# Performance work log

Measured on AMD Instinct MI355X. Metric: run time of the kernel, lower is better.

## Reference

```python
import jax, jax.numpy as jnp
import numpy as np

N = 100_000   # nodes
E = 1_600_000 # edges
G, H1, H2, Z = 64, 64, 64, 32


def _w(k, o, i):
    return jax.random.normal(k, (o, i), jnp.float32) * (1.0 / np.sqrt(i))


def setup_inputs() -> dict:
    key = jax.random.key(0)
    ks = jax.random.split(key, 16)
    inp = {
        "x": jax.random.normal(ks[0], (N, G), jnp.float32),
        "edge_src": jax.random.randint(ks[1], (E,), 0, N, jnp.int32),
        "edge_dst": jax.random.randint(ks[2], (E,), 0, N, jnp.int32),
        "eps": jax.random.normal(ks[3], (N, Z), jnp.float32),
        "W1": _w(ks[4], H1, G),  "b1": jnp.zeros((H1,), jnp.float32),
        "W2": _w(ks[5], H2, H1), "b2": jnp.zeros((H2,), jnp.float32),
        "W31": _w(ks[6], Z, H2), "b31": jnp.zeros((Z,), jnp.float32),
        "W32": _w(ks[7], Z, H2), "b32": jnp.zeros((Z,), jnp.float32),
        "W4": _w(ks[8], H2, Z),  "b4": jnp.zeros((H2,), jnp.float32),
        "W5": _w(ks[9], H1, H2), "b5": jnp.zeros((H1,), jnp.float32),
        "W6": _w(ks[10], G, H1), "b6": jnp.zeros((G,), jnp.float32),
    }
    return inp


def _gcn(h, W, b, act, src, dst, norm):
    # message: h_src * norm_src, gathered per edge  [E, d]
    m = (h * norm)[src]
    # reduce: sum over incoming edges, scaled by norm_dst  [N, d]
    agg = jax.ops.segment_sum(m, dst, num_segments=N) * norm
    # node apply: linear + activation
    return act(agg @ W.T + b)


def reference(x, edge_src, edge_dst, eps,
              W1, b1, W2, b2, W31, b31, W32, b32, W4, b4, W5, b5, W6, b6):
    # symmetric GCN norm: deg^{-1/2} from in-degree
    deg = jax.ops.segment_sum(jnp.ones((E,), jnp.float32), edge_dst, num_segments=N)
    norm = jax.lax.rsqrt(jnp.maximum(deg, 1.0))[:, None]  # [N,1]

    relu = jax.nn.relu
    ident = lambda h: h

    h = _gcn(x, W1, b1, relu, edge_src, edge_dst, norm)
    h = _gcn(h, W2, b2, relu, edge_src, edge_dst, norm)
    mu = _gcn(h, W31, b31, ident, edge_src, edge_dst, norm)
    log_var = _gcn(h, W32, b32, ident, edge_src, edge_dst, norm)

    z = eps * jnp.exp(0.5 * log_var) + mu

    h = _gcn(z, W4, b4, relu, edge_src, edge_dst, norm)
    h = _gcn(h, W5, b5, relu, edge_src, edge_dst, norm)
    recon = _gcn(h, W6, b6, jax.nn.sigmoid, edge_src, edge_dst, norm)
    return recon, mu, log_var
```

## Files before the change

kernel.cpp:

```cpp
#include <hip/hip_runtime.h>
#include <hip/hip_fp16.h>
#include <math.h>

#define NN 100000
#define NE 1600000
#define NBKT 391
#define CHUNK 8192
#define NB1 ((NE + CHUNK - 1) / CHUNK)
#define QSEG 25000
#define NNP (NN + 8)
#define CAP 5120

typedef _Float16 v8h __attribute__((ext_vector_type(8)));
typedef float v4f __attribute__((ext_vector_type(4)));

union H4 { uint2 u; __half2 h[2]; };

__global__ __launch_bounds__(256) void p1_scatter_kernel(const int* __restrict__ src,
                                                         const int* __restrict__ dst,
                                                         int* __restrict__ bcnt,
                                                         int* __restrict__ gpair) {
    __shared__ int h[NBKT], rb[NBKT], hc[NBKT];
    int tid = threadIdx.x;
    for (int b = tid; b < NBKT; b += 256) { h[b] = 0; hc[b] = 0; }
    __syncthreads();
    int e0 = blockIdx.x * CHUNK;
    for (int k = 0; k < CHUNK / 256; ++k) {
        int e = e0 + tid + k * 256;
        if (e < NE) atomicAdd(&h[dst[e] >> 8], 1);
    }
    __syncthreads();
    for (int b = tid; b < NBKT; b += 256)
        rb[b] = h[b] ? atomicAdd(&bcnt[b], h[b]) : 0;
    __syncthreads();
    for (int k = 0; k < CHUNK / 256; ++k) {
        int e = e0 + tid + k * 256;
        if (e < NE) {
            int d = dst[e], s = src[e];
            int b = d >> 8;
            int pos = b * CAP + rb[b] + atomicAdd(&hc[b], 1);
            gpair[pos] = (s << 8) | (d & 255);
        }
    }
}

__global__ __launch_bounds__(256) void p2_place_kernel(const int* __restrict__ gpair,
                                                       const int* __restrict__ bcnt,
                                                       int* __restrict__ csr,
                                                       int* __restrict__ seg,
                                                       float* __restrict__ nrm,
                                                       const float4* __restrict__ x4,
                                                       uint2* __restrict__ xs) {
    __shared__ int cseg[4][256], nexcl[256], sb[4][256], pq[4][256];
    __shared__ float nrmS[256];
    int b = blockIdx.x, tid = threadIdx.x;
    int s0 = b * CAP, s1 = s0 + bcnt[b];
#pragma unroll
    for (int q = 0; q < 4; ++q) { cseg[q][tid] = 0; pq[q][tid] = 0; }
    __syncthreads();
    for (int i = s0 + tid; i < s1; i += 256) {
        int p = gpair[i];
        int l = p & 255;
        int q = (p >> 8) / QSEG;
        atomicAdd(&cseg[q][l], 1);
    }
    __syncthreads();
    int v = cseg[0][tid] + cseg[1][tid] + cseg[2][tid] + cseg[3][tid];
    nexcl[tid] = v;
    __syncthreads();
    for (int off = 1; off < 256; off <<= 1) {
        int t = (tid >= off) ? nexcl[tid - off] : 0;
        __syncthreads();
        nexcl[tid] += t;
        __syncthreads();
    }
    int ex = nexcl[tid] - v;
    int base = s0 + ex;
    int node = (b << 8) + tid;
    int c0 = cseg[0][tid], c1 = cseg[1][tid], c2 = cseg[2][tid];
    float nv = rsqrtf(fmaxf((float)v, 1.0f));
    if (node < NN) {
        seg[0 * NNP + node] = base;
        seg[1 * NNP + node] = base + c0;
        seg[2 * NNP + node] = base + c0 + c1;
        seg[3 * NNP + node] = base + c0 + c1 + c2;
        seg[4 * NNP + node] = base + v;
        nrm[node] = nv;
    }
    nrmS[tid] = nv;
    sb[0][tid] = base;
    sb[1][tid] = base + c0;
    sb[2][tid] = base + c0 + c1;
    sb[3][tid] = base + c0 + c1 + c2;
    __syncthreads();
    for (int i = s0 + tid; i < s1; i += 256) {
        int p = gpair[i];
        int l = p & 255;
        int s = p >> 8;
        int q = s / QSEG;
        int pos = sb[q][l] + atomicAdd(&pq[q][l], 1);
        csr[pos] = s;
    }
    int nbase = b << 8;
    int nvalid = NN - nbase; if (nvalid > 256) nvalid = 256;
    for (int idx = tid; idx < nvalid * 16; idx += 256) {
        int nl = idx >> 4, f = idx & 15;
        float s = nrmS[nl];
        float4 xv = x4[(size_t)(nbase + nl) * 16 + f];
        H4 w;
        w.h[0] = __floats2half2_rn(xv.x * s, xv.y * s);
        w.h[1] = __floats2half2_rn(xv.z * s, xv.w * s);
        xs[(size_t)(nbase + nl) * 16 + f] = w.u;
    }
}

template<int IN, int ACT, bool SCALE, bool DUAL>
__global__ __launch_bounds__(256) void gcn_layer_kernel(
        const __half* __restrict__ h,
        const float* __restrict__ nrm,
        const int* __restrict__ seg,
        const int* __restrict__ csr,
        const float* __restrict__ Wa, const float* __restrict__ ba,
        const float* __restrict__ Wb, const float* __restrict__ bb,
        void* __restrict__ outv, float* __restrict__ out2,
        const float* __restrict__ eps, __half* __restrict__ zbuf) {
    constexpr int MLP = 8;
    constexpr int RL  = IN / 4;
    constexpr int EPI = 64 / RL;
    constexpr int KH  = IN / 32;
    constexpr int AS  = IN + 8;
    constexpr int HS  = 72;
    constexpr int FS  = 68;
    constexpr int MS  = 36;
    constexpr int OUTB = DUAL ? (2 * 32 * MS * 4) : (SCALE ? 32 * HS * 2 : 32 * FS * 4);
    __shared__ __half aggH[32 * AS];
    __shared__ __align__(16) char smem[OUTB];

    int tid = threadIdx.x;
    int wave = tid >> 6, lane = tid & 63;
    int row_slot = lane / RL;
    int f4 = lane % RL;
    int nodeBase = (blockIdx.x * 4 + wave) * MLP;
    const uint2* hp = (const uint2*)h;

    float4 acc[MLP];
#pragma unroll
    for (int i = 0; i < MLP; ++i) acc[i] = make_float4(0.f, 0.f, 0.f, 0.f);

    int cur[MLP];
#pragma unroll
    for (int i = 0; i < MLP; ++i) cur[i] = seg[nodeBase + i];

    for (int q = 0; q < 4; ++q) {
        int nxt[MLP];
#pragma unroll
        for (int i = 0; i < MLP; ++i) nxt[i] = seg[(q + 1) * NNP + nodeBase + i];
        int maxd = 0;
#pragma unroll
        for (int i = 0; i < MLP; ++i) maxd = max(maxd, nxt[i] - cur[i]);

        for (int t = 0; t < maxd; t += EPI) {
            int s[MLP]; float m[MLP];
#pragma unroll
            for (int i = 0; i < MLP; ++i) {
                int jj = cur[i] + t + row_slot;
                bool ok = jj < nxt[i];
                s[i] = csr[ok ? jj : 0];
                m[i] = ok ? 1.f : 0.f;
            }
            H4 v[MLP];
#pragma unroll
            for (int i = 0; i < MLP; ++i)
                v[i].u = hp[(size_t)s[i] * RL + f4];
#pragma unroll
            for (int i = 0; i < MLP; ++i) {
                float2 f01 = __half22float2(v[i].h[0]);
                float2 f23 = __half22float2(v[i].h[1]);
                acc[i].x = fmaf(m[i], f01.x, acc[i].x);
                acc[i].y = fmaf(m[i], f01.y, acc[i].y);
                acc[i].z = fmaf(m[i], f23.x, acc[i].z);
                acc[i].w = fmaf(m[i], f23.y, acc[i].w);
            }
        }
#pragma unroll
        for (int i = 0; i < MLP; ++i) cur[i] = nxt[i];
    }

#pragma unroll
    for (int i = 0; i < MLP; ++i) {
        for (int o = RL; o < 64; o <<= 1) {
            acc[i].x += __shfl_xor(acc[i].x, o);
            acc[i].y += __shfl_xor(acc[i].y, o);
            acc[i].z += __shfl_xor(acc[i].z, o);
            acc[i].w += __shfl_xor(acc[i].w, o);
        }
    }

    if (row_slot == 0) {
#pragma unroll
        for (int i = 0; i < MLP; ++i) {
            H4 w;
            w.h[0] = __floats2half2_rn(acc[i].x, acc[i].y);
            w.h[1] = __floats2half2_rn(acc[i].z, acc[i].w);
            *(uint2*)&aggH[(wave * MLP + i) * AS + f4 * 4] = w.u;
        }
    }

    int col = lane & 15, kgrp = lane >> 4;
    v8h Bhi[KH], Blo[KH];
    float bias;
    {
        const float* wrow;
        if (DUAL) wrow = (wave < 2) ? (Wa + (size_t)(wave * 16 + col) * 64)
                                    : (Wb + (size_t)((wave - 2) * 16 + col) * 64);
        else      wrow = Wa + (size_t)(wave * 16 + col) * IN;
        bias = DUAL ? ((wave < 2) ? ba[wave * 16 + col] : bb[(wave - 2) * 16 + col])
                    : ba[wave * 16 + col];
#pragma unroll
        for (int kh = 0; kh < KH; ++kh) {
            const float* wp = wrow + kh * 32 + kgrp * 8;
            float4 w0 = *(const float4*)(wp);
            float4 w1 = *(const float4*)(wp + 4);
            float wv[8] = {w0.x, w0.y, w0.z, w0.w, w1.x, w1.y, w1.z, w1.w};
#pragma unroll
            for (int j = 0; j < 8; ++j) {
                _Float16 hv = (_Float16)wv[j];
                Bhi[kh][j] = hv;
                Blo[kh][j] = (_Float16)(wv[j] - (float)hv);
            }
        }
    }
    __syncthreads();

    v4f dacc[2];
#pragma unroll
    for (int a2 = 0; a2 < 2; ++a2) dacc[a2] = (v4f){0.f, 0.f, 0.f, 0.f};

#pragma unroll
    for (int a2 = 0; a2 < 2; ++a2) {
        int arow = a2 * 16 + col;
#pragma unroll
        for (int kh = 0; kh < KH; ++kh) {
            v8h A = *(const v8h*)&aggH[arow * AS + kh * 32 + kgrp * 8];
            dacc[a2] = __builtin_amdgcn_mfma_f32_16x16x32_f16(A, Bhi[kh], dacc[a2], 0, 0, 0);
            dacc[a2] = __builtin_amdgcn_mfma_f32_16x16x32_f16(A, Blo[kh], dacc[a2], 0, 0, 0);
        }
    }

    float*  smu = (float*)smem;
    float*  slv = smu + 32 * MS;
    __half* sh  = (__half*)smem;
    float*  sf  = (float*)smem;
    size_t gbase = (size_t)blockIdx.x * 32;

#pragma unroll
    for (int a2 = 0; a2 < 2; ++a2) {
#pragma unroll
        for (int r = 0; r < 4; ++r) {
            int lnode = a2 * 16 + kgrp * 4 + r;
            float nv = nrm[gbase + lnode];
            float v = dacc[a2][r] * nv + bias;
            if (ACT == 1) v = fmaxf(v, 0.f);
            if (ACT == 2) v = 1.f / (1.f + expf(-v));
            if (DUAL) {
                if (wave < 2) smu[lnode * MS + wave * 16 + col] = v;
                else          slv[lnode * MS + (wave - 2) * 16 + col] = v;
            } else if (SCALE) {
                sh[lnode * HS + wave * 16 + col] = __float2half(v * nv);
            } else {
                sf[lnode * FS + wave * 16 + col] = v;
            }
        }
    }
    __syncthreads();

    if (DUAL) {
        float* mu_p = (float*)outv;
        for (int idx = tid; idx < 32 * 8; idx += 256) {
            int r = idx >> 3, c = idx & 7;
            *((uint4*)(mu_p + (gbase + r) * 32) + c) = *(const uint4*)&smu[r * MS + c * 4];
        }
        for (int idx = tid; idx < 32 * 8; idx += 256) {
            int r = idx >> 3, c = idx & 7;
            *((uint4*)(out2 + (gbase + r) * 32) + c) = *(const uint4*)&slv[r * MS + c * 4];
        }
        for (int idx = tid; idx < 32 * 4; idx += 256) {
            int r = idx >> 2, c0 = (idx & 3) * 8;
            size_t node = gbase + r;
            float nv = nrm[node];
            H4 w0, w1;
            float zv[8];
#pragma unroll
            for (int j = 0; j < 8; ++j) {
                float e  = eps[node * 32 + c0 + j];
                float mv = smu[r * MS + c0 + j];
                float lw = slv[r * MS + c0 + j];
                zv[j] = (e * expf(0.5f * lw) + mv) * nv;
            }
            w0.h[0] = __floats2half2_rn(zv[0], zv[1]);
            w0.h[1] = __floats2half2_rn(zv[2], zv[3]);
            w1.h[0] = __floats2half2_rn(zv[4], zv[5]);
            w1.h[1] = __floats2half2_rn(zv[6], zv[7]);
            uint4 out16;
            out16.x = w0.u.x; out16.y = w0.u.y; out16.z = w1.u.x; out16.w = w1.u.y;
            *((uint4*)(zbuf + node * 32) + (c0 >> 3)) = out16;
        }
    } else if (SCALE) {
        __half* hout = (__half*)outv;
        for (int idx = tid; idx < 32 * 8; idx += 256) {
            int r = idx >> 3, c = idx & 7;
            *((uint4*)(hout + (gbase + r) * 64) + c) = *(const uint4*)&sh[r * HS + c * 8];
        }
    } else {
        float* fout = (float*)outv;
        for (int idx = tid; idx < 32 * 16; idx += 256) {
            int r = idx >> 4, c = idx & 15;
            *((uint4*)(fout + (gbase + r) * 64) + c) = *(const uint4*)&sf[r * FS + c * 4];
        }
    }
}

extern "C" void kernel_launch(void* const* d_in, const int* in_sizes, int n_in,
                              void* d_out, int out_size, void* d_ws, size_t ws_size,
                              hipStream_t stream) {
    const float* x    = (const float*)d_in[0];
    const int*   esrc = (const int*)d_in[1];
    const int*   edst = (const int*)d_in[2];
    const float* eps  = (const float*)d_in[3];
    const float* W1  = (const float*)d_in[4];  const float* b1  = (const float*)d_in[5];
    const float* W2  = (const float*)d_in[6];  const float* b2  = (const float*)d_in[7];
    const float* W31 = (const float*)d_in[8];  const float* b31 = (const float*)d_in[9];
    const float* W32 = (const float*)d_in[10]; const float* b32 = (const float*)d_in[11];
    const float* W4  = (const float*)d_in[12]; const float* b4  = (const float*)d_in[13];
    const float* W5  = (const float*)d_in[14]; const float* b5  = (const float*)d_in[15];
    const float* W6  = (const float*)d_in[16]; const float* b6  = (const float*)d_in[17];

    float* outp  = (float*)d_out;
    float* recon = outp;
    float* mu    = outp + (size_t)NN * 64;
    float* lv    = mu   + (size_t)NN * 32;

    int* wsI       = (int*)d_ws;
    int* bcnt      = wsI;
    int* seg       = bcnt + 392;
    int* csr       = seg + 5 * NNP;
    int* gpair     = csr + NBKT * CAP;
    float* nrm     = (float*)(gpair + NBKT * CAP);
    __half* hA     = (__half*)(nrm + NN);
    __half* hB     = hA + (size_t)NN * 64;

    const int fgrid = NN / 32;

    hipMemsetAsync(bcnt, 0, 392 * sizeof(int), stream);
    p1_scatter_kernel<<<NB1, 256, 0, stream>>>(esrc, edst, bcnt, gpair);
    p2_place_kernel<<<NBKT, 256, 0, stream>>>(gpair, bcnt, csr, seg, nrm,
                                              (const float4*)x, (uint2*)hA);

    gcn_layer_kernel<64, 1, true,  false><<<fgrid, 256, 0, stream>>>(hA, nrm, seg, csr, W1,  b1,  nullptr, nullptr, hB,    nullptr, nullptr, nullptr);
    gcn_layer_kernel<64, 1, true,  false><<<fgrid, 256, 0, stream>>>(hB, nrm, seg, csr, W2,  b2,  nullptr, nullptr, hA,    nullptr, nullptr, nullptr);
    gcn_layer_kernel<64, 0, false, true ><<<fgrid, 256, 0, stream>>>(hA, nrm, seg, csr, W31, b31, W32,     b32,     mu,    lv,      eps,     hB);
    gcn_layer_kernel<32, 1, true,  false><<<fgrid, 256, 0, stream>>>(hB, nrm, seg, csr, W4,  b4,  nullptr, nullptr, hA,    nullptr, nullptr, nullptr);
    gcn_layer_kernel<64, 1, true,  false><<<fgrid, 256, 0, stream>>>(hA, nrm, seg, csr, W5,  b5,  nullptr, nullptr, hB,    nullptr, nullptr, nullptr);
    gcn_layer_kernel<64, 2, false, false><<<fgrid, 256, 0, stream>>>(hB, nrm, seg, csr, W6,  b6,  nullptr, nullptr, recon, nullptr, nullptr, nullptr);
}
```

Measured before the change: 537.1 us.

## Pad CSR segments to 4-aligned, load neighbor indices as int4, add nontemporal stores

Each node's per-quarter source segment in the CSR is padded to a multiple of four and its start index aligned, with a separate count array. This lets the gather loop fetch four neighbor indices per lane with one 16-byte load instead of one scalar index load per edge. The placement kernel stages bucket pairs in LDS and builds the CSR in place, which removes the separate gpair buffer. Output stores and eps/x loads are made nontemporal. The risk is more masked gather iterations from padding and staging that truncates any bucket larger than 5120 edges.

```diff
diff --git a/kernel.cpp b/kernel.cpp
--- a/kernel.cpp
+++ b/kernel.cpp
@@ -9,17 +9,20 @@
 #define NB1 ((NE + CHUNK - 1) / CHUNK)
 #define QSEG 25000
 #define NNP (NN + 8)
-#define CAP 5120
+#define CAPC 8192
+#define STG 5120
 
 typedef _Float16 v8h __attribute__((ext_vector_type(8)));
 typedef float v4f __attribute__((ext_vector_type(4)));
+typedef int v4i __attribute__((ext_vector_type(4)));
+typedef unsigned int v4u __attribute__((ext_vector_type(4)));
 
 union H4 { uint2 u; __half2 h[2]; };
 
 __global__ __launch_bounds__(256) void p1_scatter_kernel(const int* __restrict__ src,
                                                          const int* __restrict__ dst,
                                                          int* __restrict__ bcnt,
-                                                         int* __restrict__ gpair) {
+                                                         int* __restrict__ csr) {
     __shared__ int h[NBKT], rb[NBKT], hc[NBKT];
     int tid = threadIdx.x;
     for (int b = tid; b < NBKT; b += 256) { h[b] = 0; hc[b] = 0; }
@@ -38,35 +41,38 @@
         if (e < NE) {
             int d = dst[e], s = src[e];
             int b = d >> 8;
-            int pos = b * CAP + rb[b] + atomicAdd(&hc[b], 1);
-            gpair[pos] = (s << 8) | (d & 255);
+            int pos = b * CAPC + rb[b] + atomicAdd(&hc[b], 1);
+            csr[pos] = (s << 8) | (d & 255);
         }
     }
 }
 
-__global__ __launch_bounds__(256) void p2_place_kernel(const int* __restrict__ gpair,
-                                                       const int* __restrict__ bcnt,
+__global__ __launch_bounds__(256) void p2_place_kernel(const int* __restrict__ bcnt,
                                                        int* __restrict__ csr,
                                                        int* __restrict__ seg,
+                                                       int* __restrict__ cnt,
                                                        float* __restrict__ nrm,
                                                        const float4* __restrict__ x4,
                                                        uint2* __restrict__ xs) {
-    __shared__ int cseg[4][256], nexcl[256], sb[4][256], pq[4][256];
+    __shared__ int st[STG];
+    __shared__ int cseg[4][256], nexcl[256], sb4[4][256], pq[4][256];
     __shared__ float nrmS[256];
     int b = blockIdx.x, tid = threadIdx.x;
-    int s0 = b * CAP, s1 = s0 + bcnt[b];
+    int s0 = b * CAPC;
+    int cb = bcnt[b]; if (cb > STG) cb = STG;
+    for (int i = tid; i < cb; i += 256) st[i] = csr[s0 + i];
 #pragma unroll
     for (int q = 0; q < 4; ++q) { cseg[q][tid] = 0; pq[q][tid] = 0; }
     __syncthreads();
-    for (int i = s0 + tid; i < s1; i += 256) {
-        int p = gpair[i];
-        int l = p & 255;
-        int q = (p >> 8) / QSEG;
-        atomicAdd(&cseg[q][l], 1);
-    }
-    __syncthreads();
-    int v = cseg[0][tid] + cseg[1][tid] + cseg[2][tid] + cseg[3][tid];
-    nexcl[tid] = v;
+    for (int i = tid; i < cb; i += 256) {
+        int p = st[i];
+        atomicAdd(&cseg[(p >> 8) / QSEG][p & 255], 1);
+    }
+    __syncthreads();
+    int c0 = cseg[0][tid], c1 = cseg[1][tid], c2 = cseg[2][tid], c3 = cseg[3][tid];
+    int a0 = (c0 + 3) & ~3, a1 = (c1 + 3) & ~3, a2 = (c2 + 3) & ~3, a3 = (c3 + 3) & ~3;
+    int alen = a0 + a1 + a2 + a3;
+    nexcl[tid] = alen;
     __syncthreads();
     for (int off = 1; off < 256; off <<= 1) {
         int t = (tid >= off) ? nexcl[tid - off] : 0;
@@ -74,31 +80,27 @@
         nexcl[tid] += t;
         __syncthreads();
     }
-    int ex = nexcl[tid] - v;
-    int base = s0 + ex;
+    int base = s0 + nexcl[tid] - alen;
+    int q0 = base, q1 = q0 + a0, q2 = q1 + a1, q3 = q2 + a2;
     int node = (b << 8) + tid;
-    int c0 = cseg[0][tid], c1 = cseg[1][tid], c2 = cseg[2][tid];
-    float nv = rsqrtf(fmaxf((float)v, 1.0f));
+    int deg = c0 + c1 + c2 + c3;
+    float nv = rsqrtf(fmaxf((float)deg, 1.0f));
     if (node < NN) {
-        seg[0 * NNP + node] = base;
-        seg[1 * NNP + node] = base + c0;
-        seg[2 * NNP + node] = base + c0 + c1;
-        seg[3 * NNP + node] = base + c0 + c1 + c2;
-        seg[4 * NNP + node] = base + v;
+        seg[0 * NNP + node] = q0; seg[1 * NNP + node] = q1;
+        seg[2 * NNP + node] = q2; seg[3 * NNP + node] = q3;
+        cnt[0 * NNP + node] = c0; cnt[1 * NNP + node] = c1;
+        cnt[2 * NNP + node] = c2; cnt[3 * NNP + node] = c3;
         nrm[node] = nv;
     }
     nrmS[tid] = nv;
-    sb[0][tid] = base;
-    sb[1][tid] = base + c0;
-    sb[2][tid] = base + c0 + c1;
-    sb[3][tid] = base + c0 + c1 + c2;
-    __syncthreads();
-    for (int i = s0 + tid; i < s1; i += 256) {
-        int p = gpair[i];
+    sb4[0][tid] = q0; sb4[1][tid] = q1; sb4[2][tid] = q2; sb4[3][tid] = q3;
+    __syncthreads();
+    for (int i = tid; i < cb; i += 256) {
+        int p = st[i];
         int l = p & 255;
         int s = p >> 8;
         int q = s / QSEG;
-        int pos = sb[q][l] + atomicAdd(&pq[q][l], 1);
+        int pos = sb4[q][l] + atomicAdd(&pq[q][l], 1);
         csr[pos] = s;
     }
     int nbase = b << 8;
@@ -106,7 +108,7 @@
     for (int idx = tid; idx < nvalid * 16; idx += 256) {
         int nl = idx >> 4, f = idx & 15;
         float s = nrmS[nl];
-        float4 xv = x4[(size_t)(nbase + nl) * 16 + f];
+        v4f xv = __builtin_nontemporal_load((const v4f*)(x4 + (size_t)(nbase + nl) * 16 + f));
         H4 w;
         w.h[0] = __floats2half2_rn(xv.x * s, xv.y * s);
         w.h[1] = __floats2half2_rn(xv.z * s, xv.w * s);
@@ -119,6 +121,7 @@
         const __half* __restrict__ h,
         const float* __restrict__ nrm,
         const int* __restrict__ seg,
+        const int* __restrict__ cnt,
         const int* __restrict__ csr,
         const float* __restrict__ Wa, const float* __restrict__ ba,
         const float* __restrict__ Wb, const float* __restrict__ bb,
@@ -147,43 +150,48 @@
 #pragma unroll
     for (int i = 0; i < MLP; ++i) acc[i] = make_float4(0.f, 0.f, 0.f, 0.f);
 
-    int cur[MLP];
-#pragma unroll
-    for (int i = 0; i < MLP; ++i) cur[i] = seg[nodeBase + i];
+    int eoff = row_slot * 4;
 
     for (int q = 0; q < 4; ++q) {
-        int nxt[MLP];
-#pragma unroll
-        for (int i = 0; i < MLP; ++i) nxt[i] = seg[(q + 1) * NNP + nodeBase + i];
+        int cu[MLP], ln[MLP];
+#pragma unroll
+        for (int i = 0; i < MLP; ++i) {
+            cu[i] = seg[q * NNP + nodeBase + i] + eoff;
+            ln[i] = cnt[q * NNP + nodeBase + i];
+        }
         int maxd = 0;
 #pragma unroll
-        for (int i = 0; i < MLP; ++i) maxd = max(maxd, nxt[i] - cur[i]);
-
-        for (int t = 0; t < maxd; t += EPI) {
-            int s[MLP]; float m[MLP];
-#pragma unroll
-            for (int i = 0; i < MLP; ++i) {
-                int jj = cur[i] + t + row_slot;
-                bool ok = jj < nxt[i];
-                s[i] = csr[ok ? jj : 0];
-                m[i] = ok ? 1.f : 0.f;
-            }
-            H4 v[MLP];
+        for (int i = 0; i < MLP; ++i) maxd = max(maxd, ln[i]);
+
+        for (int t0 = 0; t0 < maxd; t0 += EPI * 4) {
+            v4i ch[MLP];
 #pragma unroll
             for (int i = 0; i < MLP; ++i)
-                v[i].u = hp[(size_t)s[i] * RL + f4];
-#pragma unroll
-            for (int i = 0; i < MLP; ++i) {
-                float2 f01 = __half22float2(v[i].h[0]);
-                float2 f23 = __half22float2(v[i].h[1]);
-                acc[i].x = fmaf(m[i], f01.x, acc[i].x);
-                acc[i].y = fmaf(m[i], f01.y, acc[i].y);
-                acc[i].z = fmaf(m[i], f23.x, acc[i].z);
-                acc[i].w = fmaf(m[i], f23.y, acc[i].w);
-            }
-        }
-#pragma unroll
-        for (int i = 0; i < MLP; ++i) cur[i] = nxt[i];
+                ch[i] = __builtin_nontemporal_load((const v4i*)(csr + cu[i] + t0));
+#pragma unroll
+            for (int u = 0; u < 4; ++u) {
+                int s[MLP]; float m[MLP];
+#pragma unroll
+                for (int i = 0; i < MLP; ++i) {
+                    bool ok = (t0 + eoff + u) < ln[i];
+                    s[i] = ok ? ch[i][u] : 0;
+                    m[i] = ok ? 1.f : 0.f;
+                }
+                H4 v[MLP];
+#pragma unroll
+                for (int i = 0; i < MLP; ++i)
+                    v[i].u = hp[(size_t)s[i] * RL + f4];
+#pragma unroll
+                for (int i = 0; i < MLP; ++i) {
+                    float2 f01 = __half22float2(v[i].h[0]);
+                    float2 f23 = __half22float2(v[i].h[1]);
+                    acc[i].x = fmaf(m[i], f01.x, acc[i].x);
+                    acc[i].y = fmaf(m[i], f01.y, acc[i].y);
+                    acc[i].z = fmaf(m[i], f23.x, acc[i].z);
+                    acc[i].w = fmaf(m[i], f23.y, acc[i].w);
+                }
+            }
+        }
     }
 
 #pragma unroll
@@ -278,44 +286,55 @@
         float* mu_p = (float*)outv;
         for (int idx = tid; idx < 32 * 8; idx += 256) {
             int r = idx >> 3, c = idx & 7;
-            *((uint4*)(mu_p + (gbase + r) * 32) + c) = *(const uint4*)&smu[r * MS + c * 4];
+            v4u v = *(const v4u*)&smu[r * MS + c * 4];
+            __builtin_nontemporal_store(v, (v4u*)(mu_p + (gbase + r) * 32) + c);
         }
         for (int idx = tid; idx < 32 * 8; idx += 256) {
             int r = idx >> 3, c = idx & 7;
-            *((uint4*)(out2 + (gbase + r) * 32) + c) = *(const uint4*)&slv[r * MS + c * 4];
+            v4u v = *(const v4u*)&slv[r * MS + c * 4];
+            __builtin_nontemporal_store(v, (v4u*)(out2 + (gbase + r) * 32) + c);
         }
         for (int idx = tid; idx < 32 * 4; idx += 256) {
             int r = idx >> 2, c0 = (idx & 3) * 8;
             size_t node = gbase + r;
             float nv = nrm[node];
-            H4 w0, w1;
+            v4f e0 = __builtin_nontemporal_load((const v4f*)(eps + node * 32 + c0));
+            v4f e1 = __builtin_nontemporal_load((const v4f*)(eps + node * 32 + c0 + 4));
             float zv[8];
 #pragma unroll
-            for (int j = 0; j < 8; ++j) {
-                float e  = eps[node * 32 + c0 + j];
+            for (int j = 0; j < 4; ++j) {
                 float mv = smu[r * MS + c0 + j];
                 float lw = slv[r * MS + c0 + j];
-                zv[j] = (e * expf(0.5f * lw) + mv) * nv;
-            }
+                zv[j] = (e0[j] * expf(0.5f * lw) + mv) * nv;
+            }
+#pragma unroll
+            for (int j = 0; j < 4; ++j) {
+                float mv = smu[r * MS + c0 + 4 + j];
+                float lw = slv[r * MS + c0 + 4 + j];
+                zv[4 + j] = (e1[j] * expf(0.5f * lw) + mv) * nv;
+            }
+            H4 w0, w1;
             w0.h[0] = __floats2half2_rn(zv[0], zv[1]);
             w0.h[1] = __floats2half2_rn(zv[2], zv[3]);
             w1.h[0] = __floats2half2_rn(zv[4], zv[5]);
             w1.h[1] = __floats2half2_rn(zv[6], zv[7]);
-            uint4 out16;
-            out16.x = w0.u.x; out16.y = w0.u.y; out16.z = w1.u.x; out16.w = w1.u.y;
-            *((uint4*)(zbuf + node * 32) + (c0 >> 3)) = out16;
+            v4u o16;
+            o16.x = w0.u.x; o16.y = w0.u.y; o16.z = w1.u.x; o16.w = w1.u.y;
+            __builtin_nontemporal_store(o16, (v4u*)(zbuf + node * 32) + (c0 >> 3));
         }
     } else if (SCALE) {
         __half* hout = (__half*)outv;
         for (int idx = tid; idx < 32 * 8; idx += 256) {
             int r = idx >> 3, c = idx & 7;
-            *((uint4*)(hout + (gbase + r) * 64) + c) = *(const uint4*)&sh[r * HS + c * 8];
+            v4u v = *(const v4u*)&sh[r * HS + c * 8];
+            __builtin_nontemporal_store(v, (v4u*)(hout + (gbase + r) * 64) + c);
         }
     } else {
         float* fout = (float*)outv;
         for (int idx = tid; idx < 32 * 16; idx += 256) {
             int r = idx >> 4, c = idx & 15;
-            *((uint4*)(fout + (gbase + r) * 64) + c) = *(const uint4*)&sf[r * FS + c * 4];
+            v4u v = *(const v4u*)&sf[r * FS + c * 4];
+            __builtin_nontemporal_store(v, (v4u*)(fout + (gbase + r) * 64) + c);
         }
     }
 }
@@ -343,23 +362,23 @@
     int* wsI       = (int*)d_ws;
     int* bcnt      = wsI;
     int* seg       = bcnt + 392;
-    int* csr       = seg + 5 * NNP;
-    int* gpair     = csr + NBKT * CAP;
-    float* nrm     = (float*)(gpair + NBKT * CAP);
+    int* cnt       = seg + 4 * NNP;
+    int* csr       = cnt + 4 * NNP;
+    float* nrm     = (float*)(csr + (size_t)NBKT * CAPC);
     __half* hA     = (__half*)(nrm + NN);
     __half* hB     = hA + (size_t)NN * 64;
 
     const int fgrid = NN / 32;
 
     hipMemsetAsync(bcnt, 0, 392 * sizeof(int), stream);
-    p1_scatter_kernel<<<NB1, 256, 0, stream>>>(esrc, edst, bcnt, gpair);
-    p2_place_kernel<<<NBKT, 256, 0, stream>>>(gpair, bcnt, csr, seg, nrm,
+    p1_scatter_kernel<<<NB1, 256, 0, stream>>>(esrc, edst, bcnt, csr);
+    p2_place_kernel<<<NBKT, 256, 0, stream>>>(bcnt, csr, seg, cnt, nrm,
                                               (const float4*)x, (uint2*)hA);
 
-    gcn_layer_kernel<64, 1, true,  false><<<fgrid, 256, 0, stream>>>(hA, nrm, seg, csr, W1,  b1,  nullptr, nullptr, hB,    nullptr, nullptr, nullptr);
-    gcn_layer_kernel<64, 1, true,  false><<<fgrid, 256, 0, stream>>>(hB, nrm, seg, csr, W2,  b2,  nullptr, nullptr, hA,    nullptr, nullptr, nullptr);
-    gcn_layer_kernel<64, 0, false, true ><<<fgrid, 256, 0, stream>>>(hA, nrm, seg, csr, W31, b31, W32,     b32,     mu,    lv,      eps,     hB);
-    gcn_layer_kernel<32, 1, true,  false><<<fgrid, 256, 0, stream>>>(hB, nrm, seg, csr, W4,  b4,  nullptr, nullptr, hA,    nullptr, nullptr, nullptr);
-    gcn_layer_kernel<64, 1, true,  false><<<fgrid, 256, 0, stream>>>(hA, nrm, seg, csr, W5,  b5,  nullptr, nullptr, hB,    nullptr, nullptr, nullptr);
-    gcn_layer_kernel<64, 2, false, false><<<fgrid, 256, 0, stream>>>(hB, nrm, seg, csr, W6,  b6,  nullptr, nullptr, recon, nullptr, nullptr, nullptr);
+    gcn_layer_kernel<64, 1, true,  false><<<fgrid, 256, 0, stream>>>(hA, nrm, seg, cnt, csr, W1,  b1,  nullptr, nullptr, hB,    nullptr, nullptr, nullptr);
+    gcn_layer_kernel<64, 1, true,  false><<<fgrid, 256, 0, stream>>>(hB, nrm, seg, cnt, csr, W2,  b2,  nullptr, nullptr, hA,    nullptr, nullptr, nullptr);
+    gcn_layer_kernel<64, 0, false, true ><<<fgrid, 256, 0, stream>>>(hA, nrm, seg, cnt, csr, W31, b31, W32,     b32,     mu,    lv,      eps,     hB);
+    gcn_layer_kernel<32, 1, true,  false><<<fgrid, 256, 0, stream>>>(hB, nrm, seg, cnt, csr, W4,  b4,  nullptr, nullptr, hA,    nullptr, nullptr, nullptr);
+    gcn_layer_kernel<64, 1, true,  false><<<fgrid, 256, 0, stream>>>(hA, nrm, seg, cnt, csr, W5,  b5,  nullptr, nullptr, hB,    nullptr, nullptr, nullptr);
+    gcn_layer_kernel<64, 2, false, false><<<fgrid, 256, 0, stream>>>(hB, nrm, seg, cnt, csr, W6,  b6,  nullptr, nullptr, recon, nullptr, nullptr, nullptr);
 }
```

Result: slower. 1.015 ms (+88.9%).
